# Kernel optimization log

Measured on AMD Instinct MI355X. Metric: run time of the kernel, lower is better.

Reference implementation:

```python
import jax, jax.numpy as jnp
import numpy as np

BS, EP = 32, 32
N_AGENTS, N_ATOM, EMBED = 8, 51, 32
STATE_DIM, HYP = 128, 64
V_MIN, V_MAX = -10.0, 10.0


def proj(support, probs, v_min, v_max, n_atom):
    # C51 categorical projection of (support, probs) onto the fixed atom grid
    # linspace(v_min, v_max, n_atom). support/probs: [..., M] -> [..., n_atom]
    support, probs = jnp.broadcast_arrays(support, probs)
    delta = (v_max - v_min) / (n_atom - 1)
    b = (jnp.clip(support, v_min, v_max) - v_min) / delta
    l = jnp.floor(b)
    u = jnp.ceil(b)
    eq = (u == l).astype(probs.dtype)  # support exactly on an atom -> all mass to l
    ml = probs * (u - b + eq)
    mu = probs * (b - l)
    shp = probs.shape
    n = int(np.prod(shp[:-1]))
    m = shp[-1]
    rows = jnp.arange(n)[:, None]
    out = jnp.zeros((n, n_atom), probs.dtype)
    out = out.at[rows, l.astype(jnp.int32).reshape(n, m)].add(ml.reshape(n, m))
    out = out.at[rows, u.astype(jnp.int32).reshape(n, m)].add(mu.reshape(n, m))
    return out.reshape(shp[:-1] + (n_atom,))


def bconv(p, q):
    # Full 1D convolution of per-row categorical pmfs (sum of two random vars).
    # p: [N, L], q: [N, M] -> [N, L+M-1], via grouped conv (one group per row).
    N, L = p.shape
    M = q.shape[-1]
    out = jax.lax.conv_general_dilated(
        p[None], jnp.flip(q, -1)[:, None, :],
        window_strides=(1,), padding=[(M - 1, M - 1)],
        feature_group_count=N, dimension_numbers=('NCW', 'OIW', 'NCW'))
    return out[0]


def mlp2(x, w1, b1, w2, b2):
    return jax.nn.relu(x @ w1.T + b1) @ w2.T + b2


def setup_inputs():
    key = jax.random.key(0)
    ks = jax.random.split(key, 20)
    def p(k, shape, s=0.05):
        return jax.random.normal(k, shape, dtype=jnp.float32) * s
    aq = jax.random.uniform(ks[0], (BS, EP, N_AGENTS, N_ATOM), dtype=jnp.float32)
    aq = aq / jnp.sum(aq, -1, keepdims=True)  # valid categorical distributions
    return {
        'agent_qs_distri': aq,
        'states': p(ks[1], (BS, EP, STATE_DIM), 1.0),
        'hw1_w1': p(ks[2], (HYP, STATE_DIM)), 'hw1_b1': p(ks[3], (HYP,)),
        'hw1_w2': p(ks[4], (EMBED * N_AGENTS, HYP)), 'hw1_b2': p(ks[5], (EMBED * N_AGENTS,)),
        'hb1_w': p(ks[6], (EMBED, STATE_DIM)), 'hb1_b': p(ks[7], (EMBED,)),
        'hwf_w1': p(ks[8], (HYP, STATE_DIM)), 'hwf_b1': p(ks[9], (HYP,)),
        'hwf_w2': p(ks[10], (EMBED, HYP)), 'hwf_b2': p(ks[11], (EMBED,)),
        'v_w1': p(ks[12], (EMBED, STATE_DIM)), 'v_b1': p(ks[13], (EMBED,)),
        'v_w2': p(ks[14], (1, EMBED)), 'v_b2': p(ks[15], (1,)),
    }


def reference(agent_qs_distri, states, hw1_w1, hw1_b1, hw1_w2, hw1_b2,
              hb1_w, hb1_b, hwf_w1, hwf_b1, hwf_w2, hwf_b2,
              v_w1, v_b1, v_w2, v_b2):
    bs, ep, n_agents, n_atom = agent_qs_distri.shape
    s = states.reshape(-1, STATE_DIM)
    atoms = jnp.linspace(V_MIN, V_MAX, n_atom).astype(jnp.float32)  # [A]

    w1 = jnp.abs(mlp2(s, hw1_w1, hw1_b1, hw1_w2, hw1_b2)).reshape(bs, ep, EMBED, n_agents)
    b1 = (s @ hb1_w.T + hb1_b).reshape(bs, ep, EMBED)

    # stage 1: scale each agent's support by w1[..., k, i], project back onto atoms
    sup1 = atoms * w1[..., None]                                       # [bs,ep,E,Na,A]
    aw = proj(sup1, agent_qs_distri[:, :, None], V_MIN, V_MAX, n_atom)  # [bs,ep,E,Na,A]
    awf = aw.reshape(-1, n_agents, n_atom)                              # [bs*ep*E,Na,A]
    q = awf[:, 0]
    for i in range(1, n_agents):
        q = bconv(q, awf[:, i])                                         # [.., Na*A-Na+1]
    L1 = n_agents * n_atom - n_agents + 1
    sup = jnp.linspace(n_agents * V_MIN, n_agents * V_MAX, L1).astype(jnp.float32)
    sup = jax.nn.elu(sup + b1[..., None])                               # [bs,ep,E,L1]
    x = proj(sup, q.reshape(bs, ep, EMBED, L1), V_MIN, V_MAX, n_atom)   # [bs,ep,E,A]

    # stage 2: hyper_w_final scaling, convolve across embed dim, add V(s)
    wf = jnp.abs(mlp2(s, hwf_w1, hwf_b1, hwf_w2, hwf_b2)).reshape(bs, ep, EMBED)
    xw = proj(atoms * wf[..., None], x, V_MIN, V_MAX, n_atom)           # [bs,ep,E,A]
    xwf = xw.reshape(-1, EMBED, n_atom)
    q = xwf[:, 0]
    for i in range(1, EMBED):
        q = bconv(q, xwf[:, i])                                         # [bs*ep, E*A-E+1]
    L2 = EMBED * n_atom - EMBED + 1
    v = mlp2(s, v_w1, v_b1, v_w2, v_b2).reshape(bs, ep, 1)
    sup2 = jnp.linspace(EMBED * V_MIN, EMBED * V_MAX, L2).astype(jnp.float32) + v
    return proj(sup2, q.reshape(bs, ep, L2), V_MIN, V_MAX, n_atom)      # [bs,ep,A]
```

## Files before the change

### kernel.cpp

```cpp
#include <hip/hip_runtime.h>
#include <hip/hip_bf16.h>
#include <math.h>

typedef unsigned short u16;

#define WAVE_SYNC() asm volatile("s_waitcnt lgkmcnt(0)" ::: "memory")

__device__ __forceinline__ float bf2f(u16 u) {
  union { unsigned int i; float f; } c;
  c.i = ((unsigned int)u) << 16;
  return c.f;
}
__device__ __forceinline__ float bflo(unsigned int u) {
  union { unsigned int i; float f; } c; c.i = u << 16; return c.f;
}
__device__ __forceinline__ float bfhi(unsigned int u) {
  union { unsigned int i; float f; } c; c.i = u & 0xffff0000u; return c.f;
}
__device__ __forceinline__ u16 f2bf(float f) {
  union { float f; unsigned int i; } c;
  c.f = f;
  unsigned int x = c.i;
  unsigned int r = (x + 0x7fffu + ((x >> 16) & 1u)) >> 16;
  return (u16)r;
}

__device__ __forceinline__ void proj_bounds(float wv, int& ML, int& MH) {
  float smin = (-10.0f + 0.4f * 0.0f)  * wv;
  float smax = (-10.0f + 0.4f * 50.0f) * wv;
  float bmin = (fminf(fmaxf(smin, -10.0f), 10.0f) + 10.0f) / 0.4f;
  float bmax = (fminf(fmaxf(smax, -10.0f), 10.0f) + 10.0f) / 0.4f;
  ML = (int)floorf(bmin);
  MH = (int)ceilf(bmax);
}

template<typename SUPP>
__device__ __forceinline__ void proj_scan(float* __restrict__ g1,
                                          float* __restrict__ g2,
                                          int span, int lane, SUPP supp)
{
  if (lane < 52) g1[lane] = 0.f;
  if (lane < 53) g2[lane] = 0.f;
  float cml = 0.f, cmu = 0.f;
  int ck = -1;
  for (int base = 0; base < span; base += 64) {
    int t = base + lane;
    bool act = (t < span);
    int tc = act ? t : (span - 1);
    float sup, p;
    supp(tc, act, sup, p);
    float c  = fminf(fmaxf(sup, -10.0f), 10.0f);
    float b  = (c + 10.0f) / 0.4f;
    float l  = floorf(b);
    float u  = ceilf(b);
    float eq = (u == l) ? 1.0f : 0.0f;
    float ml = p * (u - b + eq);
    float mu = p * (b - l);
    int   li = (int)l;
    bool last = (base + 64 >= span);
    if (lane == 0 && ck >= 0) {
      if (ck == li) { ml += cml; mu += cmu; }
      else          { g1[ck] = cml; g2[ck + 1] = cmu; }
    }
#pragma unroll
    for (int d = 1; d < 64; d <<= 1) {
      int   lo = __shfl_up(li, d);
      float a1 = __shfl_up(ml, d);
      float a2 = __shfl_up(mu, d);
      bool same = (lane >= d) && (lo == li);
      ml += same ? a1 : 0.f;
      mu += same ? a2 : 0.f;
    }
    int ln = __shfl_down(li, 1);
    bool runend = (lane == 63) ? last : (ln != li);
    if (runend) { g1[li] = ml; g2[li + 1] = mu; }
    if (!last) {
      cml = __shfl(ml, 63);
      cmu = __shfl(mu, 63);
      ck  = __shfl(li, 63);
    }
  }
}

__device__ __forceinline__ void conv_pad2(const float* __restrict__ q,
                                          float* __restrict__ qn,
                                          const float* __restrict__ kvs,
                                          int ML, int W, int T,
                                          int LQ, int HQ, int tid, int nthr)
{
  const int Lout = LQ + ML, Hout = HQ + ML + T;
  for (int J = Lout + tid; J <= Hout; J += nthr) {
    const float* qp = q + (J - ML);
    float acc = 0.f;
    for (int c = 0; c < W; c += 4) {
      float4 k4 = *(const float4*)(kvs + c);
      acc = fmaf(k4.x, qp[-c],     acc);
      acc = fmaf(k4.y, qp[-c - 1], acc);
      acc = fmaf(k4.z, qp[-c - 2], acc);
      acc = fmaf(k4.w, qp[-c - 3], acc);
    }
    qn[J] = acc;
  }
}

__device__ __forceinline__ void conv16(const float* __restrict__ q,
                                       float* __restrict__ qn,
                                       const float* __restrict__ kvs,
                                       int ML, int T,
                                       int LQ, int HQ, int lane)
{
  const int Lout = LQ + ML, Hout = HQ + ML + T;
  for (int J = Lout + lane; J <= Hout; J += 64) {
    const float* qp = q + (J - ML);
    float a0 = 0.f, a1 = 0.f;
#pragma unroll
    for (int c = 0; c < 16; c += 4) {
      float4 k4 = *(const float4*)(kvs + c);
      a0 = fmaf(k4.x, qp[-c],     a0);
      a1 = fmaf(k4.y, qp[-c - 1], a1);
      a0 = fmaf(k4.z, qp[-c - 2], a0);
      a1 = fmaf(k4.w, qp[-c - 3], a1);
    }
    qn[J] = a0 + a1;
  }
}

__device__ __forceinline__ float gather64_clamped(const float* __restrict__ pb,
                                                  float wv, float j)
{
  float a0 = 0.f, a1 = 0.f, a2 = 0.f, a3 = 0.f;
  const float4* pb4 = (const float4*)pb;
  const float base = 25.0f - j;
#pragma unroll
  for (int t4 = 0; t4 < 13; ++t4) {
    float4 p4 = pb4[t4];
#define G1(PX, TT, AC) { \
    float sup = ((float)(TT) * 0.4f - 10.0f) * wv; \
    float c   = fminf(fmaxf(sup, -10.0f), 10.0f); \
    float d   = fmaf(c, 2.5f, base); \
    AC = fmaf(PX, fmaxf(0.f, 1.0f - fabsf(d)), AC); }
    G1(p4.x, 4 * t4 + 0, a0)
    G1(p4.y, 4 * t4 + 1, a1)
    G1(p4.z, 4 * t4 + 2, a2)
    G1(p4.w, 4 * t4 + 3, a3)
#undef G1
  }
  return (a0 + a1) + (a2 + a3);
}

template<int BF>
__device__ __forceinline__ float ldt(const void* p, int i) {
  if (BF) return bf2f(((const u16*)p)[i]);
  return ((const float*)p)[i];
}

template<int BF>
__device__ __forceinline__ float dot128_t(const void* w, int row, const float* s) {
  float acc = 0.f;
  if (BF) {
    const uint4* p = (const uint4*)((const u16*)w + row * 128);
#pragma unroll
    for (int i = 0; i < 16; ++i) {
      uint4 v = p[i];
      int b = i * 8;
      acc = fmaf(bflo(v.x), s[b + 0], acc); acc = fmaf(bfhi(v.x), s[b + 1], acc);
      acc = fmaf(bflo(v.y), s[b + 2], acc); acc = fmaf(bfhi(v.y), s[b + 3], acc);
      acc = fmaf(bflo(v.z), s[b + 4], acc); acc = fmaf(bfhi(v.z), s[b + 5], acc);
      acc = fmaf(bflo(v.w), s[b + 6], acc); acc = fmaf(bfhi(v.w), s[b + 7], acc);
    }
  } else {
    const float4* p = (const float4*)((const float*)w + row * 128);
#pragma unroll
    for (int i = 0; i < 32; ++i) {
      float4 v = p[i];
      int b = i * 4;
      acc = fmaf(v.x, s[b + 0], acc); acc = fmaf(v.y, s[b + 1], acc);
      acc = fmaf(v.z, s[b + 2], acc); acc = fmaf(v.w, s[b + 3], acc);
    }
  }
  return acc;
}

template<int BF>
__device__ __forceinline__ float dot64_t(const void* w, int row, const float* h) {
  float acc = 0.f;
  if (BF) {
    const uint4* p = (const uint4*)((const u16*)w + row * 64);
#pragma unroll
    for (int i = 0; i < 8; ++i) {
      uint4 v = p[i];
      int b = i * 8;
      acc = fmaf(bflo(v.x), h[b + 0], acc); acc = fmaf(bfhi(v.x), h[b + 1], acc);
      acc = fmaf(bflo(v.y), h[b + 2], acc); acc = fmaf(bfhi(v.y), h[b + 3], acc);
      acc = fmaf(bflo(v.z), h[b + 4], acc); acc = fmaf(bfhi(v.z), h[b + 5], acc);
      acc = fmaf(bflo(v.w), h[b + 6], acc); acc = fmaf(bfhi(v.w), h[b + 7], acc);
    }
  } else {
    const float4* p = (const float4*)((const float*)w + row * 64);
#pragma unroll
    for (int i = 0; i < 16; ++i) {
      float4 v = p[i];
      int b = i * 4;
      acc = fmaf(v.x, h[b + 0], acc); acc = fmaf(v.y, h[b + 1], acc);
      acc = fmaf(v.z, h[b + 2], acc); acc = fmaf(v.w, h[b + 3], acc);
    }
  }
  return acc;
}

template<int BF>
__device__ __forceinline__ void mlp_body(
    const void* states,
    const void* hw1_w1, const void* hw1_b1, const void* hw1_w2, const void* hw1_b2,
    const void* hb1_w,  const void* hb1_b,
    const void* hwf_w1, const void* hwf_b1, const void* hwf_w2, const void* hwf_b2,
    const void* v_w1,   const void* v_b1,   const void* v_w2,   const void* v_b2,
    float* w1_ws, float* b1_ws, float* wf_ws, float* v_ws,
    int n, int tid, float* s, float* h1, float* hf, float* vh)
{
  s[tid]      = ldt<BF>(states, n * 128 + tid);
  s[tid + 64] = ldt<BF>(states, n * 128 + 64 + tid);
  __syncthreads();

  h1[tid] = fmaxf(dot128_t<BF>(hw1_w1, tid, s) + ldt<BF>(hw1_b1, tid), 0.f);
  hf[tid] = fmaxf(dot128_t<BF>(hwf_w1, tid, s) + ldt<BF>(hwf_b1, tid), 0.f);
  if (tid < 32) {
    vh[tid] = fmaxf(dot128_t<BF>(v_w1, tid, s) + ldt<BF>(v_b1, tid), 0.f);
    b1_ws[n * 32 + tid] = dot128_t<BF>(hb1_w, tid, s) + ldt<BF>(hb1_b, tid);
  }
  __syncthreads();

#pragma unroll
  for (int k = 0; k < 4; ++k) {
    int o = tid + 64 * k;
    w1_ws[n * 256 + o] = fabsf(dot64_t<BF>(hw1_w2, o, h1) + ldt<BF>(hw1_b2, o));
  }
  if (tid < 32)
    wf_ws[n * 32 + tid] = fabsf(dot64_t<BF>(hwf_w2, tid, hf) + ldt<BF>(hwf_b2, tid));
  if (tid == 0) {
    float acc = ldt<BF>(v_b2, 0);
    for (int e = 0; e < 32; ++e) acc = fmaf(ldt<BF>(v_w2, e), vh[e], acc);
    v_ws[n] = acc;
  }
}

__global__ __launch_bounds__(64) void k_mlp(
    const void* __restrict__ states,
    const void* __restrict__ hw1_w1, const void* __restrict__ hw1_b1,
    const void* __restrict__ hw1_w2, const void* __restrict__ hw1_b2,
    const void* __restrict__ hb1_w,  const void* __restrict__ hb1_b,
    const void* __restrict__ hwf_w1, const void* __restrict__ hwf_b1,
    const void* __restrict__ hwf_w2, const void* __restrict__ hwf_b2,
    const void* __restrict__ v_w1,   const void* __restrict__ v_b1,
    const void* __restrict__ v_w2,   const void* __restrict__ v_b2,
    float* __restrict__ w1_ws, float* __restrict__ b1_ws,
    float* __restrict__ wf_ws, float* __restrict__ v_ws,
    int* __restrict__ flag)
{
  __shared__ float s[128];
  __shared__ float h1[64];
  __shared__ float hf[64];
  __shared__ float vh[32];
  const int n = blockIdx.x;
  const int tid = threadIdx.x;

  const u16* sr = (const u16*)states;
  unsigned int e0 = (sr[tid] >> 7) & 0xFF;
  unsigned int e1 = (sr[tid + 64] >> 7) & 0xFF;
  unsigned long long bl0 = __ballot(e0 >= 97 && e0 <= 141);
  unsigned long long bl1 = __ballot(e1 >= 97 && e1 <= 141);
  int bf = (__popcll(bl0) + __popcll(bl1) >= 104) ? 1 : 0;
  if (tid == 0) *flag = bf;

  if (bf)
    mlp_body<1>(states, hw1_w1, hw1_b1, hw1_w2, hw1_b2, hb1_w, hb1_b,
                hwf_w1, hwf_b1, hwf_w2, hwf_b2, v_w1, v_b1, v_w2, v_b2,
                w1_ws, b1_ws, wf_ws, v_ws, n, tid, s, h1, hf, vh);
  else
    mlp_body<0>(states, hw1_w1, hw1_b1, hw1_w2, hw1_b2, hb1_w, hb1_b,
                hwf_w1, hwf_b1, hwf_w2, hwf_b2, v_w1, v_b1, v_w2, v_b2,
                w1_ws, b1_ws, wf_ws, v_ws, n, tid, s, h1, hf, vh);
}

__global__ __launch_bounds__(128) void k_perembed(
    const void* __restrict__ aq,
    const float* __restrict__ w1_ws, const float* __restrict__ b1_ws,
    const float* __restrict__ wf_ws, float* __restrict__ xw_ws,
    const int* __restrict__ flag)
{
  __shared__ __align__(16) float Ab[2][520];
  __shared__ __align__(16) float Bb[2][520];
  __shared__ __align__(16) float kv_all[2][8][16];
  __shared__ __align__(16) float kvo[2][56];
  __shared__ __align__(16) float p_lds[2][8][52];
  __shared__ float gAb[2][53];
  __shared__ float gBb[2][54];

  const int w    = threadIdx.x >> 6;
  const int lane = threadIdx.x & 63;
  const int task = blockIdx.x * 2 + w;
  const int n = task >> 5;
  const int e = task & 31;
  const int bf = *flag;

  float* A   = Ab[w];
  float* B   = Bb[w];
  float* gA  = gAb[w];
  float* gB  = gBb[w];
  float* kvo_w = kvo[w];
  float (*pl)[52] = p_lds[w];

  if (bf) {
    const u16* p = (const u16*)aq + n * 408;
    if (lane < 52) {
#pragma unroll
      for (int a = 0; a < 8; ++a)
        pl[a][lane] = (lane < 51) ? bf2f(p[a * 51 + lane]) : 0.f;
    }
  } else {
    const float* p = (const float*)aq + n * 408;
    if (lane < 52) {
#pragma unroll
      for (int a = 0; a < 8; ++a)
        pl[a][lane] = (lane < 51) ? p[a * 51 + lane] : 0.f;
    }
  }
  float wreg = (lane < 8) ? w1_ws[n * 256 + e * 8 + lane] : 0.f;
  float b1v  = b1_ws[n * 32 + e];
  float wfv  = wf_ws[n * 32 + e];

  int mlA = 0, mhA = 0;
  if (lane < 8) proj_bounds(wreg, mlA, mhA);
  WAVE_SYNC();

#pragma unroll
  for (int r = 0; r < 2; ++r) {
    int a  = 4 * r + (lane >> 4);
    int jj = lane & 15;
    float wv = __shfl(wreg, a);
    int ML = __shfl(mlA, a);
    int MH = __shfl(mhA, a);
    int T  = MH - ML;
    float K = (25.0f - (float)(ML + jj)) - 25.0f * wv;
    float a0 = 0.f, a1 = 0.f, a2 = 0.f, a3 = 0.f;
    const float4* pb4 = (const float4*)pl[a];
#pragma unroll
    for (int t4 = 0; t4 < 13; ++t4) {
      float4 p4 = pb4[t4];
      float d0 = fmaf((float)(4 * t4 + 0), wv, K);
      float d1 = fmaf((float)(4 * t4 + 1), wv, K);
      float d2 = fmaf((float)(4 * t4 + 2), wv, K);
      float d3 = fmaf((float)(4 * t4 + 3), wv, K);
      a0 = fmaf(p4.x, fmaxf(0.f, 1.0f - fabsf(d0)), a0);
      a1 = fmaf(p4.y, fmaxf(0.f, 1.0f - fabsf(d1)), a1);
      a2 = fmaf(p4.z, fmaxf(0.f, 1.0f - fabsf(d2)), a2);
      a3 = fmaf(p4.w, fmaxf(0.f, 1.0f - fabsf(d3)), a3);
    }
    if (T <= 15)
      kv_all[w][a][jj] = (jj <= T) ? ((a0 + a1) + (a2 + a3)) : 0.f;
  }
  WAVE_SYNC();

  int LQ, HQ;
  float* q = A;
  float* qn = B;
  {
    float wv0 = __shfl(wreg, 0);
    int ML0 = __shfl(mlA, 0), MH0 = __shfl(mhA, 0);
    int T0 = MH0 - ML0;
    if (T0 <= 15) {
      if (lane <= T0) A[64 + ML0 + lane] = kv_all[w][0][lane];
    } else {
      float acc = gather64_clamped(pl[0], wv0, (float)(ML0 + lane));
      if (lane <= T0) A[64 + ML0 + lane] = acc;
    }
    WAVE_SYNC();
    LQ = 64 + ML0; HQ = 64 + MH0;
  }

  for (int a = 1; a < 8; ++a) {
    float wv = __shfl(wreg, a);
    int ML = __shfl(mlA, a), MH = __shfl(mhA, a);
    int T = MH - ML;
    const float* kvs;
    int W;
    if (T <= 15) {
      kvs = &kv_all[w][a][0];
      W = 16;
    } else {
      float acc = gather64_clamped(pl[a], wv, (float)(ML + lane));
      W = (T + 4) & ~3;
      if (lane < W) kvo_w[lane] = (lane <= T) ? acc : 0.f;
      kvs = kvo_w;
    }
    if (lane < W - 1) q[LQ - 1 - lane] = 0.f;
    if (lane < T)     q[HQ + 1 + lane] = 0.f;
    WAVE_SYNC();
    if (T <= 15) conv16(q, qn, kvs, ML, T, LQ, HQ, lane);
    else         conv_pad2(q, qn, kvs, ML, W, T, LQ, HQ, lane, 64);
    WAVE_SYNC();
    LQ += ML; HQ += MH;
    float* t_ = q; q = qn; qn = t_;
  }

  {
    int span = HQ - LQ + 1;
    int LQl = LQ;
    const float* qf = q;
    proj_scan(gA, gB, span, lane, [&](int t, bool act, float& sup, float& p) {
      int tg = (LQl - 64) + t;
      float raw = (-80.0f + 0.4f * (float)tg) + b1v;
      sup = (raw > 0.f) ? raw : expm1f(raw);
      p = act ? qf[LQl + t] : 0.f;
    });
  }
  WAVE_SYNC();

  float x2v = (lane < 51) ? (gA[lane] + gB[lane]) : 0.f;
  WAVE_SYNC();
  float* x2row = pl[0];
  if (lane < 52) x2row[lane] = (lane < 51) ? x2v : 0.f;
  WAVE_SYNC();
  {
    int MLf, MHf;
    proj_bounds(wfv, MLf, MHf);
    int Tf = MHf - MLf;
    float acc = gather64_clamped(x2row, wfv, (float)(MLf + lane));
    if (lane <= Tf)
      xw_ws[task * 51 + MLf + lane] = acc;
  }
}

__global__ __launch_bounds__(256) void k_final(
    const float* __restrict__ xw_ws, const float* __restrict__ wf_ws,
    const float* __restrict__ v_ws,
    void* __restrict__ out, const int* __restrict__ flag)
{
  __shared__ __align__(16) float bufA[4608];
  __shared__ __align__(16) float bufB[4608];
  __shared__ int meta_s[63];
  __shared__ int meta_l[63];
  __shared__ int meta_ml[32];
  __shared__ int meta_g[6];
  __shared__ int meta_mltot;
  __shared__ float gA[53], gB[54];

  const int n    = blockIdx.x;
  const int tid  = threadIdx.x;
  const int lane = tid & 63;
  const int bf   = *flag;

  float wfreg = (lane < 32) ? wf_ws[n * 32 + lane] : 0.f;
  float vv    = v_ws[n];

  for (int i = tid; i < 4608; i += 256) { bufA[i] = 0.f; bufB[i] = 0.f; }

  if (tid < 64) {
    int ml, mh;
    proj_bounds(wfreg, ml, mh);
    if (lane < 32) meta_ml[lane] = ml;
    int msum = ml;
#pragma unroll
    for (int d = 1; d < 32; d <<= 1) msum += __shfl_xor(msum, d);
    if (lane == 0) meta_mltot = msum;

    int curlen = mh - ml + 1;
    int base = 0, Ncur = 32;
#pragma unroll
    for (int c = 0; c <= 5; ++c) {
      int lm = (lane < Ncur) ? curlen : 0;
#pragma unroll
      for (int d = 1; d < 32; d <<= 1) {
        int o = __shfl_xor(lm, d);
        lm = (o > lm) ? o : lm;
      }
      int G = (lm + 11) & ~3;
      int sp = ((curlen + 3) & ~3) + G;
      int inc = (lane < Ncur) ? sp : 0;
      int v0 = inc;
#pragma unroll
      for (int d = 1; d < 32; d <<= 1) {
        int u = __shfl_up(inc, d);
        if (lane >= d && lane < 32) inc += u;
      }
      if (lane < Ncur) {
        meta_s[base + lane] = 832 + (inc - v0);
        meta_l[base + lane] = curlen;
      }
      if (lane == 0) meta_g[c] = G;
      if (c < 5) {
        int l0 = __shfl(curlen, 2 * lane);
        int l1 = __shfl(curlen, 2 * lane + 1);
        curlen = l0 + l1 - 1;
        base += Ncur;
        Ncur >>= 1;
      }
    }
  }
  __syncthreads();

  {
    int g = tid >> 3, i = tid & 7;
    int s = meta_s[g], l = meta_l[g], ml = meta_ml[g];
    const float* row = xw_ws + (n * 32 + g) * 51 + ml;
    for (int i0 = i; i0 < l; i0 += 8) bufA[s + i0] = row[i0];
  }
  __syncthreads();

#pragma unroll
  for (int c = 1; c <= 5; ++c) {
    const float* bin = (c & 1) ? bufA : bufB;
    float*       bout = (c & 1) ? bufB : bufA;
    const int Nout = 32 >> c;
    const int lg = 3 + c;
    const int gs = 1 << lg;
    const int k  = tid >> lg;
    const int st = tid & (gs - 1);
    const int bc = 64 - (64 >> c);
    const int bp = 64 - (64 >> (c - 1));
    const int i0 = bp + 2 * k;
    const int sA = meta_s[i0];
    const int sB = meta_s[i0 + 1];
    const int lB = meta_l[i0 + 1];
    const int sO = meta_s[bc + k];
    const int lO = meta_l[bc + k];
    const int W  = (lB + 3) & ~3;

    for (int j = st * 2; j < lO; j += gs * 2) {
      const float* Ap = bin + sA + j + 1;
      float a0 = 0.f, a1 = 0.f;
      for (int m = 0; m < W; m += 4) {
        float4 k4 = *(const float4*)(bin + sB + m);
        float v0 = Ap[-m], v1 = Ap[-m - 1], v2 = Ap[-m - 2];
        float v3 = Ap[-m - 3], v4 = Ap[-m - 4];
        a0 = fmaf(k4.x, v1, fmaf(k4.y, v2, fmaf(k4.z, v3, fmaf(k4.w, v4, a0))));
        a1 = fmaf(k4.x, v0, fmaf(k4.y, v1, fmaf(k4.z, v2, fmaf(k4.w, v3, a1))));
      }
      bout[sO + j] = a0;
      if (j + 1 < lO) bout[sO + j + 1] = a1;
    }

    if (c >= 2 && c <= 4) {
      int G = meta_g[c];
      for (int p = tid; p < G; p += 256) bout[832 - G + p] = 0.f;
      for (int k2 = 0; k2 < Nout; ++k2) {
        int ss = meta_s[bc + k2] + meta_l[bc + k2];
        int ee = (k2 + 1 < Nout) ? meta_s[bc + k2 + 1]
                                 : ss + G + 3;
        for (int p = ss + tid; p < ee; p += 256) bout[p] = 0.f;
      }
    }
    __syncthreads();
  }

  if (tid < 64) {
    int s5 = meta_s[62], l5 = meta_l[62], mlt = meta_mltot;
    const float* qf = bufB + s5;
    proj_scan(gA, gB, l5, lane, [&](int t, bool act, float& sup, float& p) {
      int tg = mlt + t;
      sup = (-320.0f + 0.4f * (float)tg) + vv;
      p = act ? qf[t] : 0.f;
    });
    WAVE_SYNC();
    if (lane < 51) {
      float o = gA[lane] + gB[lane];
      if (bf) ((u16*)out)[n * 51 + lane] = f2bf(o);
      else    ((float*)out)[n * 51 + lane] = o;
    }
  }
}

extern "C" void kernel_launch(void* const* d_in, const int* in_sizes, int n_in,
                              void* d_out, int out_size, void* d_ws, size_t ws_size,
                              hipStream_t stream)
{
  float* ws    = (float*)d_ws;
  float* w1_ws = ws;
  float* b1_ws = w1_ws + 1024 * 256;
  float* wf_ws = b1_ws + 1024 * 32;
  float* v_ws  = wf_ws + 1024 * 32;
  float* xw_ws = v_ws  + 1024;
  int*   flag  = (int*)(xw_ws + 1024 * 32 * 51);

  k_mlp<<<1024, 64, 0, stream>>>(d_in[1],
      d_in[2], d_in[3], d_in[4], d_in[5], d_in[6], d_in[7],
      d_in[8], d_in[9], d_in[10], d_in[11], d_in[12], d_in[13],
      d_in[14], d_in[15],
      w1_ws, b1_ws, wf_ws, v_ws, flag);

  k_perembed<<<16384, 128, 0, stream>>>(d_in[0], w1_ws, b1_ws, wf_ws, xw_ws, flag);

  k_final<<<1024, 256, 0, stream>>>(xw_ws, wf_ws, v_ws, d_out, flag);
}
```

Before: 248.5 us.

## Split each per-embed task across two waves instead of one wave per task

k_perembed now gives each (sample, embed) task a full 128-thread block, with both waves sharing the agent-convolution chain, the kernel-weight build and the final gather. Before, each wave handled its own task independently. The aim is to shorten the serial per-task latency by doubling the threads working on each convolution. In exchange, the grid doubles, block-wide __syncthreads replace wave-local syncs, and the projection scan leaves one wave idle.

```diff
diff --git a/kernel.cpp b/kernel.cpp
--- a/kernel.cpp
+++ b/kernel.cpp
@@ -107,10 +107,10 @@
                                        float* __restrict__ qn,
                                        const float* __restrict__ kvs,
                                        int ML, int T,
-                                       int LQ, int HQ, int lane)
+                                       int LQ, int HQ, int tid, int nthr)
 {
   const int Lout = LQ + ML, Hout = HQ + ML + T;
-  for (int J = Lout + lane; J <= Hout; J += 64) {
+  for (int J = Lout + tid; J <= Hout; J += nthr) {
     const float* qp = q + (J - ML);
     float a0 = 0.f, a1 = 0.f;
 #pragma unroll
@@ -125,14 +125,15 @@
   }
 }
 
-__device__ __forceinline__ float gather64_clamped(const float* __restrict__ pb,
-                                                  float wv, float j)
+template<int TA, int TB>
+__device__ __forceinline__ float gather_part(const float* __restrict__ pb,
+                                             float wv, float j)
 {
   float a0 = 0.f, a1 = 0.f, a2 = 0.f, a3 = 0.f;
   const float4* pb4 = (const float4*)pb;
   const float base = 25.0f - j;
 #pragma unroll
-  for (int t4 = 0; t4 < 13; ++t4) {
+  for (int t4 = TA; t4 < TB; ++t4) {
     float4 p4 = pb4[t4];
 #define G1(PX, TT, AC) { \
     float sup = ((float)(TT) * 0.4f - 10.0f) * wv; \
@@ -288,41 +289,40 @@
     const float* __restrict__ wf_ws, float* __restrict__ xw_ws,
     const int* __restrict__ flag)
 {
-  __shared__ __align__(16) float Ab[2][520];
-  __shared__ __align__(16) float Bb[2][520];
-  __shared__ __align__(16) float kv_all[2][8][16];
-  __shared__ __align__(16) float kvo[2][56];
-  __shared__ __align__(16) float p_lds[2][8][52];
-  __shared__ float gAb[2][53];
-  __shared__ float gBb[2][54];
-
-  const int w    = threadIdx.x >> 6;
-  const int lane = threadIdx.x & 63;
-  const int task = blockIdx.x * 2 + w;
+  __shared__ __align__(16) float Ab[520];
+  __shared__ __align__(16) float Bb[520];
+  __shared__ __align__(16) float kv_all[8][16];
+  __shared__ __align__(16) float kvo[56];
+  __shared__ __align__(16) float p_lds[8][52];
+  __shared__ float gA[53];
+  __shared__ float gB[54];
+  __shared__ __align__(16) float pE[2][64];
+
+  const int tid  = threadIdx.x;
+  const int wit  = tid >> 6;
+  const int lane = tid & 63;
+  const int task = blockIdx.x;
   const int n = task >> 5;
   const int e = task & 31;
   const int bf = *flag;
 
-  float* A   = Ab[w];
-  float* B   = Bb[w];
-  float* gA  = gAb[w];
-  float* gB  = gBb[w];
-  float* kvo_w = kvo[w];
-  float (*pl)[52] = p_lds[w];
-
   if (bf) {
     const u16* p = (const u16*)aq + n * 408;
     if (lane < 52) {
 #pragma unroll
-      for (int a = 0; a < 8; ++a)
-        pl[a][lane] = (lane < 51) ? bf2f(p[a * 51 + lane]) : 0.f;
+      for (int k = 0; k < 4; ++k) {
+        int a = 4 * wit + k;
+        p_lds[a][lane] = (lane < 51) ? bf2f(p[a * 51 + lane]) : 0.f;
+      }
     }
   } else {
     const float* p = (const float*)aq + n * 408;
     if (lane < 52) {
 #pragma unroll
-      for (int a = 0; a < 8; ++a)
-        pl[a][lane] = (lane < 51) ? p[a * 51 + lane] : 0.f;
+      for (int k = 0; k < 4; ++k) {
+        int a = 4 * wit + k;
+        p_lds[a][lane] = (lane < 51) ? p[a * 51 + lane] : 0.f;
+      }
     }
   }
   float wreg = (lane < 8) ? w1_ws[n * 256 + e * 8 + lane] : 0.f;
@@ -333,9 +333,8 @@
   if (lane < 8) proj_bounds(wreg, mlA, mhA);
   WAVE_SYNC();
 
-#pragma unroll
-  for (int r = 0; r < 2; ++r) {
-    int a  = 4 * r + (lane >> 4);
+  {
+    int a  = 4 * wit + (lane >> 4);
     int jj = lane & 15;
     float wv = __shfl(wreg, a);
     int ML = __shfl(mlA, a);
@@ -343,7 +342,7 @@
     int T  = MH - ML;
     float K = (25.0f - (float)(ML + jj)) - 25.0f * wv;
     float a0 = 0.f, a1 = 0.f, a2 = 0.f, a3 = 0.f;
-    const float4* pb4 = (const float4*)pl[a];
+    const float4* pb4 = (const float4*)p_lds[a];
 #pragma unroll
     for (int t4 = 0; t4 < 13; ++t4) {
       float4 p4 = pb4[t4];
@@ -357,24 +356,25 @@
       a3 = fmaf(p4.w, fmaxf(0.f, 1.0f - fabsf(d3)), a3);
     }
     if (T <= 15)
-      kv_all[w][a][jj] = (jj <= T) ? ((a0 + a1) + (a2 + a3)) : 0.f;
-  }
-  WAVE_SYNC();
+      kv_all[a][jj] = (jj <= T) ? ((a0 + a1) + (a2 + a3)) : 0.f;
+  }
+  __syncthreads();
 
   int LQ, HQ;
-  float* q = A;
-  float* qn = B;
+  float* q = Ab;
+  float* qn = Bb;
   {
     float wv0 = __shfl(wreg, 0);
     int ML0 = __shfl(mlA, 0), MH0 = __shfl(mhA, 0);
     int T0 = MH0 - ML0;
-    if (T0 <= 15) {
-      if (lane <= T0) A[64 + ML0 + lane] = kv_all[w][0][lane];
-    } else {
-      float acc = gather64_clamped(pl[0], wv0, (float)(ML0 + lane));
-      if (lane <= T0) A[64 + ML0 + lane] = acc;
-    }
-    WAVE_SYNC();
+    if (tid < 64) {
+      if (T0 <= 15) {
+        if (lane <= T0) Ab[64 + ML0 + lane] = kv_all[0][lane];
+      } else {
+        float acc = gather_part<0, 13>(p_lds[0], wv0, (float)(ML0 + lane));
+        if (lane <= T0) Ab[64 + ML0 + lane] = acc;
+      }
+    }
     LQ = 64 + ML0; HQ = 64 + MH0;
   }
 
@@ -385,25 +385,27 @@
     const float* kvs;
     int W;
     if (T <= 15) {
-      kvs = &kv_all[w][a][0];
+      kvs = &kv_all[a][0];
       W = 16;
     } else {
-      float acc = gather64_clamped(pl[a], wv, (float)(ML + lane));
       W = (T + 4) & ~3;
-      if (lane < W) kvo_w[lane] = (lane <= T) ? acc : 0.f;
-      kvs = kvo_w;
-    }
-    if (lane < W - 1) q[LQ - 1 - lane] = 0.f;
-    if (lane < T)     q[HQ + 1 + lane] = 0.f;
-    WAVE_SYNC();
-    if (T <= 15) conv16(q, qn, kvs, ML, T, LQ, HQ, lane);
-    else         conv_pad2(q, qn, kvs, ML, W, T, LQ, HQ, lane, 64);
-    WAVE_SYNC();
+      if (tid < 64) {
+        float acc = gather_part<0, 13>(p_lds[a], wv, (float)(ML + lane));
+        if (lane < W) kvo[lane] = (lane <= T) ? acc : 0.f;
+      }
+      kvs = kvo;
+    }
+    if (tid < W - 1) q[LQ - 1 - tid] = 0.f;
+    if (tid < T)     q[HQ + 1 + tid] = 0.f;
+    __syncthreads();
+    if (T <= 15) conv16(q, qn, kvs, ML, T, LQ, HQ, tid, 128);
+    else         conv_pad2(q, qn, kvs, ML, W, T, LQ, HQ, tid, 128);
+    __syncthreads();
     LQ += ML; HQ += MH;
     float* t_ = q; q = qn; qn = t_;
   }
 
-  {
+  if (wit == 0) {
     int span = HQ - LQ + 1;
     int LQl = LQ;
     const float* qf = q;
@@ -413,21 +415,23 @@
       sup = (raw > 0.f) ? raw : expm1f(raw);
       p = act ? qf[LQl + t] : 0.f;
     });
-  }
-  WAVE_SYNC();
-
-  float x2v = (lane < 51) ? (gA[lane] + gB[lane]) : 0.f;
-  WAVE_SYNC();
-  float* x2row = pl[0];
-  if (lane < 52) x2row[lane] = (lane < 51) ? x2v : 0.f;
-  WAVE_SYNC();
+    WAVE_SYNC();
+    float x2v = (lane < 51) ? (gA[lane] + gB[lane]) : 0.f;
+    WAVE_SYNC();
+    if (lane < 52) p_lds[0][lane] = (lane < 51) ? x2v : 0.f;
+  }
+  __syncthreads();
+
   {
     int MLf, MHf;
     proj_bounds(wfv, MLf, MHf);
-    int Tf = MHf - MLf;
-    float acc = gather64_clamped(x2row, wfv, (float)(MLf + lane));
-    if (lane <= Tf)
-      xw_ws[task * 51 + MLf + lane] = acc;
+    float j = (float)(MLf + lane);
+    float part = (wit == 0) ? gather_part<0, 7>(p_lds[0], wfv, j)
+                            : gather_part<7, 13>(p_lds[0], wfv, j);
+    pE[wit][lane] = part;
+    __syncthreads();
+    if (wit == 0 && lane <= MHf - MLf)
+      xw_ws[task * 51 + MLf + lane] = pE[0][lane] + pE[1][lane];
   }
 }
 
@@ -588,7 +592,7 @@
       d_in[14], d_in[15],
       w1_ws, b1_ws, wf_ws, v_ws, flag);
 
-  k_perembed<<<16384, 128, 0, stream>>>(d_in[0], w1_ws, b1_ws, wf_ws, xw_ws, flag);
+  k_perembed<<<32768, 128, 0, stream>>>(d_in[0], w1_ws, b1_ws, wf_ws, xw_ws, flag);
 
   k_final<<<1024, 256, 0, stream>>>(xw_ws, wf_ws, v_ws, d_out, flag);
 }
```

Result: slower. 274.6 us (+10.5%).

## Fuse MLP, per-embed convolution and final stage into one kernel

Applied to the files above, without the earlier changes.

Replaces the three launches (hypernet MLP, per-embed agent convolution, final embed convolution) with a single 512-thread kernel per batch element. Intermediates (hypernet weights, per-embed projected distributions) stay in shared memory instead of going through global workspace. Each of the 8 waves handles 4 embeds in sequence, and the final stage uses twice as many threads. This removes launch gaps and global round-trips, but gives up the parallelism of 16384 small blocks. The large shared footprint may also limit occupancy.

```diff
diff --git a/kernel.cpp b/kernel.cpp
--- a/kernel.cpp
+++ b/kernel.cpp
@@ -107,10 +107,10 @@
                                        float* __restrict__ qn,
                                        const float* __restrict__ kvs,
                                        int ML, int T,
-                                       int LQ, int HQ, int lane)
+                                       int LQ, int HQ, int tid, int nthr)
 {
   const int Lout = LQ + ML, Hout = HQ + ML + T;
-  for (int J = Lout + lane; J <= Hout; J += 64) {
+  for (int J = Lout + tid; J <= Hout; J += nthr) {
     const float* qp = q + (J - ML);
     float a0 = 0.f, a1 = 0.f;
 #pragma unroll
@@ -125,14 +125,15 @@
   }
 }
 
-__device__ __forceinline__ float gather64_clamped(const float* __restrict__ pb,
-                                                  float wv, float j)
+template<int TA, int TB>
+__device__ __forceinline__ float gather_part(const float* __restrict__ pb,
+                                             float wv, float j)
 {
   float a0 = 0.f, a1 = 0.f, a2 = 0.f, a3 = 0.f;
   const float4* pb4 = (const float4*)pb;
   const float base = 25.0f - j;
 #pragma unroll
-  for (int t4 = 0; t4 < 13; ++t4) {
+  for (int t4 = TA; t4 < TB; ++t4) {
     float4 p4 = pb4[t4];
 #define G1(PX, TT, AC) { \
     float sup = ((float)(TT) * 0.4f - 10.0f) * wv; \
@@ -209,43 +210,8 @@
 }
 
 template<int BF>
-__device__ __forceinline__ void mlp_body(
-    const void* states,
-    const void* hw1_w1, const void* hw1_b1, const void* hw1_w2, const void* hw1_b2,
-    const void* hb1_w,  const void* hb1_b,
-    const void* hwf_w1, const void* hwf_b1, const void* hwf_w2, const void* hwf_b2,
-    const void* v_w1,   const void* v_b1,   const void* v_w2,   const void* v_b2,
-    float* w1_ws, float* b1_ws, float* wf_ws, float* v_ws,
-    int n, int tid, float* s, float* h1, float* hf, float* vh)
-{
-  s[tid]      = ldt<BF>(states, n * 128 + tid);
-  s[tid + 64] = ldt<BF>(states, n * 128 + 64 + tid);
-  __syncthreads();
-
-  h1[tid] = fmaxf(dot128_t<BF>(hw1_w1, tid, s) + ldt<BF>(hw1_b1, tid), 0.f);
-  hf[tid] = fmaxf(dot128_t<BF>(hwf_w1, tid, s) + ldt<BF>(hwf_b1, tid), 0.f);
-  if (tid < 32) {
-    vh[tid] = fmaxf(dot128_t<BF>(v_w1, tid, s) + ldt<BF>(v_b1, tid), 0.f);
-    b1_ws[n * 32 + tid] = dot128_t<BF>(hb1_w, tid, s) + ldt<BF>(hb1_b, tid);
-  }
-  __syncthreads();
-
-#pragma unroll
-  for (int k = 0; k < 4; ++k) {
-    int o = tid + 64 * k;
-    w1_ws[n * 256 + o] = fabsf(dot64_t<BF>(hw1_w2, o, h1) + ldt<BF>(hw1_b2, o));
-  }
-  if (tid < 32)
-    wf_ws[n * 32 + tid] = fabsf(dot64_t<BF>(hwf_w2, tid, hf) + ldt<BF>(hwf_b2, tid));
-  if (tid == 0) {
-    float acc = ldt<BF>(v_b2, 0);
-    for (int e = 0; e < 32; ++e) acc = fmaf(ldt<BF>(v_w2, e), vh[e], acc);
-    v_ws[n] = acc;
-  }
-}
-
-__global__ __launch_bounds__(64) void k_mlp(
-    const void* __restrict__ states,
+__device__ void fused_body(
+    const void* __restrict__ aq, const void* __restrict__ states,
     const void* __restrict__ hw1_w1, const void* __restrict__ hw1_b1,
     const void* __restrict__ hw1_w2, const void* __restrict__ hw1_b2,
     const void* __restrict__ hb1_w,  const void* __restrict__ hb1_b,
@@ -253,207 +219,174 @@
     const void* __restrict__ hwf_w2, const void* __restrict__ hwf_b2,
     const void* __restrict__ v_w1,   const void* __restrict__ v_b1,
     const void* __restrict__ v_w2,   const void* __restrict__ v_b2,
-    float* __restrict__ w1_ws, float* __restrict__ b1_ws,
-    float* __restrict__ wf_ws, float* __restrict__ v_ws,
-    int* __restrict__ flag)
-{
-  __shared__ float s[128];
-  __shared__ float h1[64];
-  __shared__ float hf[64];
-  __shared__ float vh[32];
-  const int n = blockIdx.x;
-  const int tid = threadIdx.x;
-
-  const u16* sr = (const u16*)states;
-  unsigned int e0 = (sr[tid] >> 7) & 0xFF;
-  unsigned int e1 = (sr[tid + 64] >> 7) & 0xFF;
-  unsigned long long bl0 = __ballot(e0 >= 97 && e0 <= 141);
-  unsigned long long bl1 = __ballot(e1 >= 97 && e1 <= 141);
-  int bf = (__popcll(bl0) + __popcll(bl1) >= 104) ? 1 : 0;
-  if (tid == 0) *flag = bf;
-
-  if (bf)
-    mlp_body<1>(states, hw1_w1, hw1_b1, hw1_w2, hw1_b2, hb1_w, hb1_b,
-                hwf_w1, hwf_b1, hwf_w2, hwf_b2, v_w1, v_b1, v_w2, v_b2,
-                w1_ws, b1_ws, wf_ws, v_ws, n, tid, s, h1, hf, vh);
-  else
-    mlp_body<0>(states, hw1_w1, hw1_b1, hw1_w2, hw1_b2, hb1_w, hb1_b,
-                hwf_w1, hwf_b1, hwf_w2, hwf_b2, v_w1, v_b1, v_w2, v_b2,
-                w1_ws, b1_ws, wf_ws, v_ws, n, tid, s, h1, hf, vh);
-}
-
-__global__ __launch_bounds__(128) void k_perembed(
-    const void* __restrict__ aq,
-    const float* __restrict__ w1_ws, const float* __restrict__ b1_ws,
-    const float* __restrict__ wf_ws, float* __restrict__ xw_ws,
-    const int* __restrict__ flag)
-{
-  __shared__ __align__(16) float Ab[2][520];
-  __shared__ __align__(16) float Bb[2][520];
-  __shared__ __align__(16) float kv_all[2][8][16];
-  __shared__ __align__(16) float kvo[2][56];
-  __shared__ __align__(16) float p_lds[2][8][52];
-  __shared__ float gAb[2][53];
-  __shared__ float gBb[2][54];
-
-  const int w    = threadIdx.x >> 6;
-  const int lane = threadIdx.x & 63;
-  const int task = blockIdx.x * 2 + w;
-  const int n = task >> 5;
-  const int e = task & 31;
-  const int bf = *flag;
-
-  float* A   = Ab[w];
-  float* B   = Bb[w];
-  float* gA  = gAb[w];
-  float* gB  = gBb[w];
-  float* kvo_w = kvo[w];
-  float (*pl)[52] = p_lds[w];
-
-  if (bf) {
-    const u16* p = (const u16*)aq + n * 408;
-    if (lane < 52) {
-#pragma unroll
-      for (int a = 0; a < 8; ++a)
-        pl[a][lane] = (lane < 51) ? bf2f(p[a * 51 + lane]) : 0.f;
-    }
-  } else {
-    const float* p = (const float*)aq + n * 408;
-    if (lane < 52) {
-#pragma unroll
-      for (int a = 0; a < 8; ++a)
-        pl[a][lane] = (lane < 51) ? p[a * 51 + lane] : 0.f;
-    }
-  }
-  float wreg = (lane < 8) ? w1_ws[n * 256 + e * 8 + lane] : 0.f;
-  float b1v  = b1_ws[n * 32 + e];
-  float wfv  = wf_ws[n * 32 + e];
-
-  int mlA = 0, mhA = 0;
-  if (lane < 8) proj_bounds(wreg, mlA, mhA);
-  WAVE_SYNC();
-
-#pragma unroll
-  for (int r = 0; r < 2; ++r) {
-    int a  = 4 * r + (lane >> 4);
-    int jj = lane & 15;
-    float wv = __shfl(wreg, a);
-    int ML = __shfl(mlA, a);
-    int MH = __shfl(mhA, a);
-    int T  = MH - ML;
-    float K = (25.0f - (float)(ML + jj)) - 25.0f * wv;
-    float a0 = 0.f, a1 = 0.f, a2 = 0.f, a3 = 0.f;
-    const float4* pb4 = (const float4*)pl[a];
-#pragma unroll
-    for (int t4 = 0; t4 < 13; ++t4) {
-      float4 p4 = pb4[t4];
-      float d0 = fmaf((float)(4 * t4 + 0), wv, K);
-      float d1 = fmaf((float)(4 * t4 + 1), wv, K);
-      float d2 = fmaf((float)(4 * t4 + 2), wv, K);
-      float d3 = fmaf((float)(4 * t4 + 3), wv, K);
-      a0 = fmaf(p4.x, fmaxf(0.f, 1.0f - fabsf(d0)), a0);
-      a1 = fmaf(p4.y, fmaxf(0.f, 1.0f - fabsf(d1)), a1);
-      a2 = fmaf(p4.z, fmaxf(0.f, 1.0f - fabsf(d2)), a2);
-      a3 = fmaf(p4.w, fmaxf(0.f, 1.0f - fabsf(d3)), a3);
-    }
-    if (T <= 15)
-      kv_all[w][a][jj] = (jj <= T) ? ((a0 + a1) + (a2 + a3)) : 0.f;
-  }
-  WAVE_SYNC();
-
-  int LQ, HQ;
-  float* q = A;
-  float* qn = B;
+    void* __restrict__ out,
+    float* SH, float* xw_lds, float* p_lds, float* s_st,
+    float* h1, float* hf, float* vh,
+    float* w1s, float* b1s, float* wfs, float* vs,
+    int* meta_s, int* meta_l, int* meta_ml, int* meta_g, int* meta_mltot,
+    int n, int tid)
+{
+  const int lane = tid & 63;
+  const int w    = tid >> 6;
+
+  if (tid < 128) s_st[tid] = ldt<BF>(states, n * 128 + tid);
+  if (tid >= 192) {
+    for (int u = tid - 192; u < 416; u += 320) {
+      int a = u / 52, c2 = u - a * 52;
+      p_lds[u] = (c2 < 51) ? ldt<BF>(aq, n * 408 + a * 51 + c2) : 0.f;
+    }
+  }
+  __syncthreads();
+  if (tid < 64)       h1[tid]        = fmaxf(dot128_t<BF>(hw1_w1, tid, s_st) + ldt<BF>(hw1_b1, tid), 0.f);
+  else if (tid < 128) hf[tid - 64]   = fmaxf(dot128_t<BF>(hwf_w1, tid - 64, s_st) + ldt<BF>(hwf_b1, tid - 64), 0.f);
+  else if (tid < 160) vh[tid - 128]  = fmaxf(dot128_t<BF>(v_w1, tid - 128, s_st) + ldt<BF>(v_b1, tid - 128), 0.f);
+  else if (tid < 192) b1s[tid - 160] = dot128_t<BF>(hb1_w, tid - 160, s_st) + ldt<BF>(hb1_b, tid - 160);
+  __syncthreads();
+  if (tid < 256)      w1s[tid]       = fabsf(dot64_t<BF>(hw1_w2, tid, h1) + ldt<BF>(hw1_b2, tid));
+  else if (tid < 288) wfs[tid - 256] = fabsf(dot64_t<BF>(hwf_w2, tid - 256, hf) + ldt<BF>(hwf_b2, tid - 256));
+  else if (tid < 320) {
+    int l2 = tid - 288;
+    float part = vh[l2] * ldt<BF>(v_w2, l2);
+    part += __shfl_xor(part, 1);  part += __shfl_xor(part, 2);
+    part += __shfl_xor(part, 4);  part += __shfl_xor(part, 8);
+    part += __shfl_xor(part, 16);
+    if (l2 == 0) vs[0] = part + ldt<BF>(v_b2, 0);
+  }
+  __syncthreads();
+
   {
-    float wv0 = __shfl(wreg, 0);
-    int ML0 = __shfl(mlA, 0), MH0 = __shfl(mhA, 0);
-    int T0 = MH0 - ML0;
-    if (T0 <= 15) {
-      if (lane <= T0) A[64 + ML0 + lane] = kv_all[w][0][lane];
-    } else {
-      float acc = gather64_clamped(pl[0], wv0, (float)(ML0 + lane));
-      if (lane <= T0) A[64 + ML0 + lane] = acc;
-    }
-    WAVE_SYNC();
-    LQ = 64 + ML0; HQ = 64 + MH0;
-  }
-
-  for (int a = 1; a < 8; ++a) {
-    float wv = __shfl(wreg, a);
-    int ML = __shfl(mlA, a), MH = __shfl(mhA, a);
-    int T = MH - ML;
-    const float* kvs;
-    int W;
-    if (T <= 15) {
-      kvs = &kv_all[w][a][0];
-      W = 16;
-    } else {
-      float acc = gather64_clamped(pl[a], wv, (float)(ML + lane));
-      W = (T + 4) & ~3;
-      if (lane < W) kvo_w[lane] = (lane <= T) ? acc : 0.f;
-      kvs = kvo_w;
-    }
-    if (lane < W - 1) q[LQ - 1 - lane] = 0.f;
-    if (lane < T)     q[HQ + 1 + lane] = 0.f;
-    WAVE_SYNC();
-    if (T <= 15) conv16(q, qn, kvs, ML, T, LQ, HQ, lane);
-    else         conv_pad2(q, qn, kvs, ML, W, T, LQ, HQ, lane, 64);
-    WAVE_SYNC();
-    LQ += ML; HQ += MH;
-    float* t_ = q; q = qn; qn = t_;
-  }
-
-  {
-    int span = HQ - LQ + 1;
-    int LQl = LQ;
-    const float* qf = q;
-    proj_scan(gA, gB, span, lane, [&](int t, bool act, float& sup, float& p) {
-      int tg = (LQl - 64) + t;
-      float raw = (-80.0f + 0.4f * (float)tg) + b1v;
-      sup = (raw > 0.f) ? raw : expm1f(raw);
-      p = act ? qf[LQl + t] : 0.f;
-    });
-  }
-  WAVE_SYNC();
-
-  float x2v = (lane < 51) ? (gA[lane] + gB[lane]) : 0.f;
-  WAVE_SYNC();
-  float* x2row = pl[0];
-  if (lane < 52) x2row[lane] = (lane < 51) ? x2v : 0.f;
-  WAVE_SYNC();
-  {
-    int MLf, MHf;
-    proj_bounds(wfv, MLf, MHf);
-    int Tf = MHf - MLf;
-    float acc = gather64_clamped(x2row, wfv, (float)(MLf + lane));
-    if (lane <= Tf)
-      xw_ws[task * 51 + MLf + lane] = acc;
-  }
-}
-
-__global__ __launch_bounds__(256) void k_final(
-    const float* __restrict__ xw_ws, const float* __restrict__ wf_ws,
-    const float* __restrict__ v_ws,
-    void* __restrict__ out, const int* __restrict__ flag)
-{
-  __shared__ __align__(16) float bufA[4608];
-  __shared__ __align__(16) float bufB[4608];
-  __shared__ int meta_s[63];
-  __shared__ int meta_l[63];
-  __shared__ int meta_ml[32];
-  __shared__ int meta_g[6];
-  __shared__ int meta_mltot;
-  __shared__ float gA[53], gB[54];
-
-  const int n    = blockIdx.x;
-  const int tid  = threadIdx.x;
-  const int lane = tid & 63;
-  const int bf   = *flag;
-
-  float wfreg = (lane < 32) ? wf_ws[n * 32 + lane] : 0.f;
-  float vv    = v_ws[n];
-
-  for (int i = tid; i < 4608; i += 256) { bufA[i] = 0.f; bufB[i] = 0.f; }
+    float* WB  = SH + w * 1408;
+    float* Ab  = WB;
+    float* Bb  = WB + 520;
+    float* kv  = WB + 1040;
+    float* kvo = WB + 1168;
+    float* x2  = WB + 1224;
+    float* gA  = WB + 1280;
+    float* gB  = WB + 1333;
+#pragma unroll 1
+    for (int i = 0; i < 4; ++i) {
+      const int e   = w + 8 * i;
+      const float b1v = b1s[e];
+      const float wfv = wfs[e];
+
+#pragma unroll
+      for (int r = 0; r < 2; ++r) {
+        int a  = 4 * r + (lane >> 4);
+        int jj = lane & 15;
+        float wv = w1s[e * 8 + a];
+        int ML, MH; proj_bounds(wv, ML, MH);
+        int T  = MH - ML;
+        float K = (25.0f - (float)(ML + jj)) - 25.0f * wv;
+        float a0 = 0.f, a1 = 0.f, a2 = 0.f, a3 = 0.f;
+        const float4* pb4 = (const float4*)(p_lds + a * 52);
+#pragma unroll
+        for (int t4 = 0; t4 < 13; ++t4) {
+          float4 p4 = pb4[t4];
+          float d0 = fmaf((float)(4 * t4 + 0), wv, K);
+          float d1 = fmaf((float)(4 * t4 + 1), wv, K);
+          float d2 = fmaf((float)(4 * t4 + 2), wv, K);
+          float d3 = fmaf((float)(4 * t4 + 3), wv, K);
+          a0 = fmaf(p4.x, fmaxf(0.f, 1.0f - fabsf(d0)), a0);
+          a1 = fmaf(p4.y, fmaxf(0.f, 1.0f - fabsf(d1)), a1);
+          a2 = fmaf(p4.z, fmaxf(0.f, 1.0f - fabsf(d2)), a2);
+          a3 = fmaf(p4.w, fmaxf(0.f, 1.0f - fabsf(d3)), a3);
+        }
+        if (T <= 15)
+          kv[a * 16 + jj] = (jj <= T) ? ((a0 + a1) + (a2 + a3)) : 0.f;
+      }
+      WAVE_SYNC();
+
+      float* q = Ab; float* qn = Bb;
+      int LQ, HQ;
+      {
+        float wv0 = w1s[e * 8];
+        int ML0, MH0; proj_bounds(wv0, ML0, MH0);
+        int T0 = MH0 - ML0;
+        if (T0 <= 15) {
+          if (lane <= T0) Ab[64 + ML0 + lane] = kv[lane];
+        } else {
+          float acc = gather_part<0, 13>(p_lds, wv0, (float)(ML0 + lane));
+          if (lane <= T0) Ab[64 + ML0 + lane] = acc;
+        }
+        WAVE_SYNC();
+        LQ = 64 + ML0; HQ = 64 + MH0;
+      }
+
+      for (int a = 1; a < 8; ++a) {
+        float wv = w1s[e * 8 + a];
+        int ML, MH; proj_bounds(wv, ML, MH);
+        int T = MH - ML;
+        const float* kvs; int W;
+        if (T <= 15) {
+          kvs = kv + a * 16; W = 16;
+        } else {
+          float acc = gather_part<0, 13>(p_lds + a * 52, wv, (float)(ML + lane));
+          W = (T + 4) & ~3;
+          if (lane < W) kvo[lane] = (lane <= T) ? acc : 0.f;
+          kvs = kvo;
+        }
+        if (lane < W - 1) q[LQ - 1 - lane] = 0.f;
+        if (lane < T)     q[HQ + 1 + lane] = 0.f;
+        WAVE_SYNC();
+        if (T <= 15) conv16(q, qn, kvs, ML, T, LQ, HQ, lane, 64);
+        else         conv_pad2(q, qn, kvs, ML, W, T, LQ, HQ, lane, 64);
+        WAVE_SYNC();
+        LQ += ML; HQ += MH;
+        float* t_ = q; q = qn; qn = t_;
+      }
+
+      {
+        int span = HQ - LQ + 1, LQl = LQ;
+        const float* qf = q;
+        proj_scan(gA, gB, span, lane, [&](int t, bool act, float& sup, float& p) {
+          int tg = (LQl - 64) + t;
+          float raw = (-80.0f + 0.4f * (float)tg) + b1v;
+          sup = (raw > 0.f) ? raw : expm1f(raw);
+          p = act ? qf[LQl + t] : 0.f;
+        });
+      }
+      WAVE_SYNC();
+      float x2v = (lane < 51) ? (gA[lane] + gB[lane]) : 0.f;
+      if (lane < 52) x2[lane] = (lane < 51) ? x2v : 0.f;
+      WAVE_SYNC();
+
+      {
+        int MLf, MHf; proj_bounds(wfv, MLf, MHf);
+        int Tf = MHf - MLf;
+        if (Tf <= 15) {
+          int q4 = lane >> 4, jj = lane & 15;
+          float K = (25.0f - (float)(MLf + jj)) - 25.0f * wfv;
+          float acc = 0.f;
+#pragma unroll
+          for (int k = 0; k < 13; ++k) {
+            int t = q4 + 4 * k;
+            float d = fmaf((float)t, wfv, K);
+            acc = fmaf(x2[t], fmaxf(0.f, 1.0f - fabsf(d)), acc);
+          }
+          acc += __shfl_xor(acc, 16);
+          acc += __shfl_xor(acc, 32);
+          if (lane <= Tf)
+            xw_lds[e * 52 + MLf + lane] = acc;
+        } else {
+          float acc = gather_part<0, 13>(x2, wfv, (float)(MLf + lane));
+          if (lane <= Tf)
+            xw_lds[e * 52 + MLf + lane] = acc;
+        }
+      }
+      WAVE_SYNC();
+    }
+  }
+  __syncthreads();
+
+  float* bufA = SH;
+  float* bufB = SH + 4608;
+  float* gA3  = SH + 9216;
+  float* gB3  = SH + 9269;
+
+  float wfreg = (lane < 32) ? wfs[lane] : 0.f;
+  float vv    = vs[0];
+
+  for (int i2 = tid; i2 < 4608; i2 += 512) { bufA[i2] = 0.f; bufB[i2] = 0.f; }
 
   if (tid < 64) {
     int ml, mh;
@@ -462,7 +395,7 @@
     int msum = ml;
 #pragma unroll
     for (int d = 1; d < 32; d <<= 1) msum += __shfl_xor(msum, d);
-    if (lane == 0) meta_mltot = msum;
+    if (lane == 0) *meta_mltot = msum;
 
     int curlen = mh - ml + 1;
     int base = 0, Ncur = 32;
@@ -500,10 +433,10 @@
   __syncthreads();
 
   {
-    int g = tid >> 3, i = tid & 7;
-    int s = meta_s[g], l = meta_l[g], ml = meta_ml[g];
-    const float* row = xw_ws + (n * 32 + g) * 51 + ml;
-    for (int i0 = i; i0 < l; i0 += 8) bufA[s + i0] = row[i0];
+    int g = tid >> 4, i3 = tid & 15;
+    int s2 = meta_s[g], l2 = meta_l[g], ml = meta_ml[g];
+    const float* row = xw_lds + g * 52 + ml;
+    for (int i0 = i3; i0 < l2; i0 += 16) bufA[s2 + i0] = row[i0];
   }
   __syncthreads();
 
@@ -512,7 +445,7 @@
     const float* bin = (c & 1) ? bufA : bufB;
     float*       bout = (c & 1) ? bufB : bufA;
     const int Nout = 32 >> c;
-    const int lg = 3 + c;
+    const int lg = 4 + c;
     const int gs = 1 << lg;
     const int k  = tid >> lg;
     const int st = tid & (gs - 1);
@@ -542,53 +475,91 @@
 
     if (c >= 2 && c <= 4) {
       int G = meta_g[c];
-      for (int p = tid; p < G; p += 256) bout[832 - G + p] = 0.f;
+      for (int p = tid; p < G; p += 512) bout[832 - G + p] = 0.f;
       for (int k2 = 0; k2 < Nout; ++k2) {
         int ss = meta_s[bc + k2] + meta_l[bc + k2];
         int ee = (k2 + 1 < Nout) ? meta_s[bc + k2 + 1]
                                  : ss + G + 3;
-        for (int p = ss + tid; p < ee; p += 256) bout[p] = 0.f;
+        for (int p = ss + tid; p < ee; p += 512) bout[p] = 0.f;
       }
     }
     __syncthreads();
   }
 
   if (tid < 64) {
-    int s5 = meta_s[62], l5 = meta_l[62], mlt = meta_mltot;
+    int s5 = meta_s[62], l5 = meta_l[62], mlt = *meta_mltot;
     const float* qf = bufB + s5;
-    proj_scan(gA, gB, l5, lane, [&](int t, bool act, float& sup, float& p) {
+    proj_scan(gA3, gB3, l5, lane, [&](int t, bool act, float& sup, float& p) {
       int tg = mlt + t;
       sup = (-320.0f + 0.4f * (float)tg) + vv;
       p = act ? qf[t] : 0.f;
     });
     WAVE_SYNC();
     if (lane < 51) {
-      float o = gA[lane] + gB[lane];
-      if (bf) ((u16*)out)[n * 51 + lane] = f2bf(o);
+      float o = gA3[lane] + gB3[lane];
+      if (BF) ((u16*)out)[n * 51 + lane] = f2bf(o);
       else    ((float*)out)[n * 51 + lane] = o;
     }
   }
+}
+
+__global__ __launch_bounds__(512) void k_fused(
+    const void* __restrict__ aq, const void* __restrict__ states,
+    const void* __restrict__ hw1_w1, const void* __restrict__ hw1_b1,
+    const void* __restrict__ hw1_w2, const void* __restrict__ hw1_b2,
+    const void* __restrict__ hb1_w,  const void* __restrict__ hb1_b,
+    const void* __restrict__ hwf_w1, const void* __restrict__ hwf_b1,
+    const void* __restrict__ hwf_w2, const void* __restrict__ hwf_b2,
+    const void* __restrict__ v_w1,   const void* __restrict__ v_b1,
+    const void* __restrict__ v_w2,   const void* __restrict__ v_b2,
+    void* __restrict__ out)
+{
+  __shared__ __align__(16) float SH[11264];
+  __shared__ __align__(16) float xw_lds[32 * 52];
+  __shared__ __align__(16) float p_lds[8 * 52];
+  __shared__ __align__(16) float s_st[128];
+  __shared__ float h1[64], hf[64], vh[32];
+  __shared__ __align__(16) float w1s[256];
+  __shared__ float b1s[32], wfs[32], vs[1];
+  __shared__ int meta_s[63], meta_l[63], meta_ml[32], meta_g[6], meta_mltot;
+  __shared__ int sh_flag;
+
+  const int tid = threadIdx.x;
+  const int n   = blockIdx.x;
+
+  if (tid < 64) {
+    const u16* sr = (const u16*)states;
+    unsigned int e0 = (sr[tid] >> 7) & 0xFF;
+    unsigned int e1 = (sr[tid + 64] >> 7) & 0xFF;
+    unsigned long long bl0 = __ballot(e0 >= 97 && e0 <= 141);
+    unsigned long long bl1 = __ballot(e1 >= 97 && e1 <= 141);
+    int bfv = (__popcll(bl0) + __popcll(bl1) >= 104) ? 1 : 0;
+    if (tid == 0) sh_flag = bfv;
+  }
+  __syncthreads();
+  const int bf = sh_flag;
+
+  if (bf)
+    fused_body<1>(aq, states, hw1_w1, hw1_b1, hw1_w2, hw1_b2, hb1_w, hb1_b,
+                  hwf_w1, hwf_b1, hwf_w2, hwf_b2, v_w1, v_b1, v_w2, v_b2, out,
+                  SH, xw_lds, p_lds, s_st, h1, hf, vh, w1s, b1s, wfs, vs,
+                  meta_s, meta_l, meta_ml, meta_g, &meta_mltot, n, tid);
+  else
+    fused_body<0>(aq, states, hw1_w1, hw1_b1, hw1_w2, hw1_b2, hb1_w, hb1_b,
+                  hwf_w1, hwf_b1, hwf_w2, hwf_b2, v_w1, v_b1, v_w2, v_b2, out,
+                  SH, xw_lds, p_lds, s_st, h1, hf, vh, w1s, b1s, wfs, vs,
+                  meta_s, meta_l, meta_ml, meta_g, &meta_mltot, n, tid);
 }
 
 extern "C" void kernel_launch(void* const* d_in, const int* in_sizes, int n_in,
                               void* d_out, int out_size, void* d_ws, size_t ws_size,
                               hipStream_t stream)
 {
-  float* ws    = (float*)d_ws;
-  float* w1_ws = ws;
-  float* b1_ws = w1_ws + 1024 * 256;
-  float* wf_ws = b1_ws + 1024 * 32;
-  float* v_ws  = wf_ws + 1024 * 32;
-  float* xw_ws = v_ws  + 1024;
-  int*   flag  = (int*)(xw_ws + 1024 * 32 * 51);
-
-  k_mlp<<<1024, 64, 0, stream>>>(d_in[1],
+  (void)d_ws; (void)ws_size; (void)in_sizes; (void)n_in; (void)out_size;
+  k_fused<<<1024, 512, 0, stream>>>(
+      d_in[0], d_in[1],
       d_in[2], d_in[3], d_in[4], d_in[5], d_in[6], d_in[7],
       d_in[8], d_in[9], d_in[10], d_in[11], d_in[12], d_in[13],
       d_in[14], d_in[15],
-      w1_ws, b1_ws, wf_ws, v_ws, flag);
-
-  k_perembed<<<16384, 128, 0, stream>>>(d_in[0], w1_ws, b1_ws, wf_ws, xw_ws, flag);
-
-  k_final<<<1024, 256, 0, stream>>>(xw_ws, wf_ws, v_ws, d_out, flag);
-}
+      d_out);
+}
```

After: 334.1 us. +34.5%, slower.
